# Performance work log

Hardware: AMD Instinct MI355X
Metric: run time of the kernel (lower is better)

The kernel has to match this reference:

```python
import jax, jax.numpy as jnp
import numpy as np

B = 64


def _upsample_conv1x1(f, cw, cb, size):
    # bilinear upsample (align_corners=False == jax half-pixel) + 1x1 conv
    u = jax.image.resize(f, (f.shape[0], f.shape[1], size, size), method='bilinear')
    return jnp.einsum('bchw,oc->bohw', u, cw) + cb[None, :, None, None]


def _shuffle_byblock(x, perms, block_size):
    # Rearrange 'b c (h h1) (w w1) -> b c (h w) h1 w1', then per-block channel
    # permutation: shuffled[:, j, i] = blocks[:, perms[i, j], i], then inverse.
    Bsz, C, H, _ = x.shape
    nb = H // block_size
    blocks = x.reshape(Bsz, C, nb, block_size, nb, block_size)
    blocks = blocks.transpose(0, 1, 2, 4, 3, 5).reshape(Bsz, C, nb * nb, block_size, block_size)
    idx = perms[: nb * nb].T  # [C, nb*nb]; idx[j, i] = perms[i, j]
    shuf = jnp.take_along_axis(blocks, idx[None, :, :, None, None], axis=1)
    shuf = shuf.reshape(Bsz, C, nb, nb, block_size, block_size)
    shuf = shuf.transpose(0, 1, 2, 4, 3, 5).reshape(Bsz, C, H, H)
    return shuf


def setup_inputs() -> dict:
    key = jax.random.key(0)
    ks = jax.random.split(key, 10)
    f1 = jax.random.normal(ks[0], (B, 64, 28, 28), jnp.float32)
    f2 = jax.random.normal(ks[1], (B, 128, 14, 14), jnp.float32)
    f3 = jax.random.normal(ks[2], (B, 128, 7, 7), jnp.float32)
    f4 = jax.random.normal(ks[3], (B, 512, 7, 7), jnp.float32)
    x_final = jax.random.normal(ks[4], (B, 512), jnp.float32)
    cw1 = jax.random.normal(ks[5], (64, 64), jnp.float32) * 0.1
    cb1 = jnp.zeros((64,), jnp.float32)
    cw2 = jax.random.normal(ks[6], (128, 128), jnp.float32) * 0.1
    cb2 = jnp.zeros((128,), jnp.float32)
    cw3 = jax.random.normal(ks[7], (256, 128), jnp.float32) * 0.1
    cb3 = jnp.zeros((256,), jnp.float32)
    cw4 = jax.random.normal(ks[8], (512, 512), jnp.float32) * 0.1
    cb4 = jnp.zeros((512,), jnp.float32)
    w1 = jnp.ones((64, 56, 56), jnp.float32)
    w2 = jnp.ones((128, 28, 28), jnp.float32)
    w3 = jnp.ones((256, 14, 14), jnp.float32)
    w4 = jnp.ones((512, 7, 7), jnp.float32)
    rng = np.random.default_rng(0)
    perms = jnp.asarray(np.stack([rng.permutation(64) for _ in range(28 * 28)]).astype(np.int32))
    return dict(f1=f1, f2=f2, f3=f3, f4=f4, x_final=x_final,
                cw1=cw1, cb1=cb1, cw2=cw2, cb2=cb2, cw3=cw3, cb3=cb3, cw4=cw4, cb4=cb4,
                w1=w1, w2=w2, w3=w3, w4=w4, perms=perms)


def reference(f1, f2, f3, f4, x_final, cw1, cb1, cw2, cb2, cw3, cb3, cw4, cb4,
              w1, w2, w3, w4, perms):
    aux1 = _shuffle_byblock(_upsample_conv1x1(f1, cw1, cb1, 56), perms, 28)
    aux2 = _upsample_conv1x1(f2, cw2, cb2, 28)
    aux3 = _upsample_conv1x1(f3, cw3, cb3, 14)
    aux4 = _upsample_conv1x1(f4, cw4, cb4, 7)
    return (x_final, aux1, aux2, aux3, aux4, w1, w2, w3, w4)
```

## Files before the change

### kernel.cpp

```cpp
#include <hip/hip_runtime.h>
#include <hip/hip_bf16.h>
#include <cstddef>

typedef __attribute__((ext_vector_type(8))) short bf16x8;
typedef __attribute__((ext_vector_type(4))) float f32x4;

__device__ __forceinline__ float4 ld4(const float* p) { return *(const float4*)p; }
__device__ __forceinline__ unsigned short f2bf(float v) {
  __hip_bfloat16 h = __float2bfloat16(v);
  return *(unsigned short*)&h;
}

__device__ __forceinline__ bf16x8 pack8(float v0, float v1, float v2, float v3,
                                        float v4, float v5, float v6, float v7) {
  bf16x8 r;
  r[0] = (short)f2bf(v0); r[1] = (short)f2bf(v1);
  r[2] = (short)f2bf(v2); r[3] = (short)f2bf(v3);
  r[4] = (short)f2bf(v4); r[5] = (short)f2bf(v5);
  r[6] = (short)f2bf(v6); r[7] = (short)f2bf(v7);
  return r;
}
__device__ __forceinline__ bf16x8 cfrag(const float* __restrict__ p) {
  float4 a = ld4(p), b = ld4(p + 4);
  return pack8(a.x, a.y, a.z, a.w, b.x, b.y, b.z, b.w);
}
__device__ __forceinline__ bf16x8 gfrag(const float* __restrict__ p, int stride) {
  float v0 = p[0], v1 = p[stride], v2 = p[2 * stride], v3 = p[3 * stride];
  float v4 = p[4 * stride], v5 = p[5 * stride], v6 = p[6 * stride], v7 = p[7 * stride];
  return pack8(v0, v1, v2, v3, v4, v5, v6, v7);
}
__device__ __forceinline__ bf16x8 gfrag_guard(const float* __restrict__ p, int stride, bool ok) {
  float v0 = ok ? p[0] : 0.f, v1 = ok ? p[stride] : 0.f;
  float v2 = ok ? p[2 * stride] : 0.f, v3 = ok ? p[3 * stride] : 0.f;
  float v4 = ok ? p[4 * stride] : 0.f, v5 = ok ? p[5 * stride] : 0.f;
  float v6 = ok ? p[6 * stride] : 0.f, v7 = ok ? p[7 * stride] : 0.f;
  return pack8(v0, v1, v2, v3, v4, v5, v6, v7);
}

__device__ __forceinline__ void up_quad_rows(const float* __restrict__ s0,
                                             const float* __restrict__ s1,
                                             const float* __restrict__ s2,
                                             int qx, int W, float* __restrict__ dst, int pitch) {
  int cm = qx > 0 ? qx - 1 : 0, cp = qx < W - 1 ? qx + 1 : W - 1;
  float tA0 = 0.25f * s0[cm] + 0.75f * s0[qx], tA1 = 0.75f * s0[qx] + 0.25f * s0[cp];
  float tB0 = 0.25f * s1[cm] + 0.75f * s1[qx], tB1 = 0.75f * s1[qx] + 0.25f * s1[cp];
  float tC0 = 0.25f * s2[cm] + 0.75f * s2[qx], tC1 = 0.75f * s2[qx] + 0.25f * s2[cp];
  *(float2*)dst = make_float2(0.25f * tA0 + 0.75f * tB0, 0.25f * tA1 + 0.75f * tB1);
  *(float2*)(dst + pitch) = make_float2(0.75f * tB0 + 0.25f * tC0, 0.75f * tB1 + 0.25f * tC1);
}

__device__ __forceinline__ void up_quad2(const float* __restrict__ s0,
                                         const float* __restrict__ s1,
                                         const float* __restrict__ s2,
                                         int qx0, int W, float* __restrict__ dst, int pitch) {
  int cm = qx0 > 0 ? qx0 - 1 : 0;
  int c2 = qx0 + 2 < W ? qx0 + 2 : W - 1;
  float Am = s0[cm], A0 = s0[qx0], A1 = s0[qx0 + 1], A2 = s0[c2];
  float Bm = s1[cm], B0 = s1[qx0], B1 = s1[qx0 + 1], B2 = s1[c2];
  float Cm = s2[cm], C0 = s2[qx0], C1 = s2[qx0 + 1], C2 = s2[c2];
  float hA0 = 0.25f * Am + 0.75f * A0, hA1 = 0.75f * A0 + 0.25f * A1;
  float hA2 = 0.25f * A0 + 0.75f * A1, hA3 = 0.75f * A1 + 0.25f * A2;
  float hB0 = 0.25f * Bm + 0.75f * B0, hB1 = 0.75f * B0 + 0.25f * B1;
  float hB2 = 0.25f * B0 + 0.75f * B1, hB3 = 0.75f * B1 + 0.25f * B2;
  float hC0 = 0.25f * Cm + 0.75f * C0, hC1 = 0.75f * C0 + 0.25f * C1;
  float hC2 = 0.25f * C0 + 0.75f * C1, hC3 = 0.75f * C1 + 0.25f * C2;
  *(float4*)dst = make_float4(0.25f * hA0 + 0.75f * hB0, 0.25f * hA1 + 0.75f * hB1,
                              0.25f * hA2 + 0.75f * hB2, 0.25f * hA3 + 0.75f * hB3);
  *(float4*)(dst + pitch) = make_float4(0.75f * hB0 + 0.25f * hC0, 0.75f * hB1 + 0.25f * hC1,
                                        0.75f * hB2 + 0.25f * hC2, 0.75f * hB3 + 0.25f * hC3);
}

struct P1M { float ct[16][252]; int inv[4][16]; };
struct C2M { float ct[32][126]; };
struct C3M { float ct[64][49]; };
union SmemM { P1M p1; C2M c2; C3M c3; };

__device__ __forceinline__ int2 xcd_decode(int d, int wpb_log) {
  int xcd = d & 7;
  int i = (d >> 3) & ((1 << wpb_log) - 1);
  int b = (((d >> (3 + wpb_log)) << 3) | xcd);
  return make_int2(b, i);
}

__global__ void __launch_bounds__(256)
fused_all(const float* __restrict__ f1, const float* __restrict__ f2,
          const float* __restrict__ f3, const float* __restrict__ f4,
          const float* __restrict__ cw1, const float* __restrict__ cb1,
          const float* __restrict__ cw2, const float* __restrict__ cb2,
          const float* __restrict__ cw3, const float* __restrict__ cb3,
          const float* __restrict__ cw4, const float* __restrict__ cb4,
          const float* __restrict__ xf, const float* __restrict__ w1,
          const float* __restrict__ w2, const float* __restrict__ w3,
          const float* __restrict__ w4s, const int* __restrict__ perms,
          float* __restrict__ out) {
  __shared__ SmemM sm;
  const int raw = blockIdx.x, tid = threadIdx.x;
  const int wave = tid >> 6, lane = tid & 63;
  const int l15 = lane & 15, lg = lane >> 4;
  float* o_aux1 = out + 32768;
  float* o_aux2 = o_aux1 + 12845056;
  float* o_aux3 = o_aux2 + 6422528;
  float* o_aux4 = o_aux3 + 3211264;

  if (raw < 512) {
    int2 bi = xcd_decode(raw, 3);
    const int b = bi.x;
    const int wm = bi.y * 64 + wave * 16;
    const float* f4b = f4 + (size_t)b * 25088;

    f32x4 acc[4];
    {
      float bv0 = cb4[wm + lg * 4 + 0], bv1 = cb4[wm + lg * 4 + 1];
      float bv2 = cb4[wm + lg * 4 + 2], bv3 = cb4[wm + lg * 4 + 3];
      for (int n = 0; n < 4; ++n) {
        acc[n][0] = bv0; acc[n][1] = bv1; acc[n][2] = bv2; acc[n][3] = bv3;
      }
    }
    const float* ap = cw4 + (size_t)(wm + l15) * 512 + lg * 8;
    int poff[4]; bool pok[4];
#pragma unroll
    for (int n = 0; n < 4; ++n) {
      int p = n * 16 + l15;
      pok[n] = p < 49;
      poff[n] = pok[n] ? p : 0;
    }
#pragma unroll 2
    for (int k0 = 0; k0 < 512; k0 += 32) {
      bf16x8 A = cfrag(ap + k0);
      const float* fb = f4b + (size_t)(k0 + lg * 8) * 49;
      bf16x8 B0 = gfrag_guard(fb + poff[0], 49, pok[0]);
      bf16x8 B1 = gfrag_guard(fb + poff[1], 49, pok[1]);
      bf16x8 B2 = gfrag_guard(fb + poff[2], 49, pok[2]);
      bf16x8 B3 = gfrag_guard(fb + poff[3], 49, pok[3]);
      acc[0] = __builtin_amdgcn_mfma_f32_16x16x32_bf16(A, B0, acc[0], 0, 0, 0);
      acc[1] = __builtin_amdgcn_mfma_f32_16x16x32_bf16(A, B1, acc[1], 0, 0, 0);
      acc[2] = __builtin_amdgcn_mfma_f32_16x16x32_bf16(A, B2, acc[2], 0, 0, 0);
      acc[3] = __builtin_amdgcn_mfma_f32_16x16x32_bf16(A, B3, acc[3], 0, 0, 0);
    }
    float* outb = o_aux4 + (size_t)b * 25088;
#pragma unroll
    for (int n = 0; n < 4; ++n) {
      int p = n * 16 + l15;
      if (p < 49) {
#pragma unroll
        for (int r = 0; r < 4; ++r) {
          int o = wm + lg * 4 + r;
          outb[(size_t)o * 49 + p] = acc[n][r];
        }
      }
    }
  } else if (raw < 1536) {
    int2 bi = xcd_decode(raw - 512, 4);
    const int b = bi.x;
    const int o0 = (bi.y >> 2) * 16;
    const int r0 = (bi.y & 3) * 7, base = r0 - 1;
    const float* f1b = f1 + (size_t)b * 50176;

    if (tid >= 128 && tid < 192) {
      int t2 = tid - 128;
      int i = t2 >> 4, cl = t2 & 15;
      int c = o0 + cl;
      int r = 0;
      for (int j = 0; j < 64; ++j)
        if (perms[i * 64 + j] == c) r = j;
      sm.p1.inv[i][cl] = r;
    }

    int off[4];
#pragma unroll
    for (int j = 0; j < 4; ++j) {
      int praw = wave * 64 + j * 16 + l15;
      int p = praw < 251 ? praw : 251;
      int lr = p / 28, x = p - lr * 28;
      int sr = base + lr;
      sr = sr < 0 ? 0 : (sr > 27 ? 27 : sr);
      off[j] = sr * 28 + x;
    }
    f32x4 acc[4];
    {
      float bv0 = cb1[o0 + lg * 4 + 0], bv1 = cb1[o0 + lg * 4 + 1];
      float bv2 = cb1[o0 + lg * 4 + 2], bv3 = cb1[o0 + lg * 4 + 3];
#pragma unroll
      for (int j = 0; j < 4; ++j) {
        acc[j][0] = bv0; acc[j][1] = bv1; acc[j][2] = bv2; acc[j][3] = bv3;
      }
    }
    const float* ap = cw1 + (size_t)(o0 + l15) * 64 + lg * 8;
#pragma unroll
    for (int ks = 0; ks < 2; ++ks) {
      bf16x8 A = cfrag(ap + ks * 32);
      const float* fb = f1b + (size_t)(ks * 32 + lg * 8) * 784;
#pragma unroll
      for (int j = 0; j < 4; ++j) {
        bf16x8 B = gfrag(fb + off[j], 784);
        acc[j] = __builtin_amdgcn_mfma_f32_16x16x32_bf16(A, B, acc[j], 0, 0, 0);
      }
    }
#pragma unroll
    for (int j = 0; j < 4; ++j) {
      int praw = wave * 64 + j * 16 + l15;
      if (praw < 252) {
#pragma unroll
        for (int r = 0; r < 4; ++r) sm.p1.ct[lg * 4 + r][praw] = acc[j][r];
      }
    }
    __syncthreads();

    const size_t obase = (size_t)b * 200704;
    for (int i = tid; i < 1568; i += 256) {
      int cl = i / 98;
      int rem = i - cl * 98;
      int ly = rem / 14, pr = rem - ly * 14;
      int qx0 = 2 * pr;
      int qy = r0 + ly;
      int lr = ly + 1;
      int qi = ((qy >= 14) ? 2 : 0) + ((qx0 >= 14) ? 1 : 0);
      int j = sm.p1.inv[qi][cl];
      float* dst = o_aux1 + obase + (size_t)j * 3136 + (size_t)(2 * qy) * 56 + 2 * qx0;
      up_quad2(&sm.p1.ct[cl][(lr - 1) * 28], &sm.p1.ct[cl][lr * 28],
               &sm.p1.ct[cl][(lr + 1) * 28], qx0, 28, dst, 56);
    }
  } else if (raw < 2048) {
    int2 bi = xcd_decode(raw - 1536, 3);
    const int b = bi.x;
    const int o0 = (bi.y >> 1) * 32;
    const int r0 = (bi.y & 1) * 7, base = r0 - 1;
    const int og = wave >> 1, nt = wave & 1;
    const int om = o0 + og * 16;
    const float* f2b = f2 + (size_t)b * 25088;

    int off[4];
#pragma unroll
    for (int j = 0; j < 4; ++j) {
      int praw = nt * 64 + j * 16 + l15;
      int p = praw < 125 ? praw : 125;
      int lr = p / 14, x = p - lr * 14;
      int sr = base + lr;
      sr = sr < 0 ? 0 : (sr > 13 ? 13 : sr);
      off[j] = sr * 14 + x;
    }
    f32x4 acc[4];
    {
      float bv0 = cb2[om + lg * 4 + 0], bv1 = cb2[om + lg * 4 + 1];
      float bv2 = cb2[om + lg * 4 + 2], bv3 = cb2[om + lg * 4 + 3];
#pragma unroll
      for (int j = 0; j < 4; ++j) {
        acc[j][0] = bv0; acc[j][1] = bv1; acc[j][2] = bv2; acc[j][3] = bv3;
      }
    }
    const float* ap = cw2 + (size_t)(om + l15) * 128 + lg * 8;
#pragma unroll
    for (int ks = 0; ks < 4; ++ks) {
      bf16x8 A = cfrag(ap + ks * 32);
      const float* fb = f2b + (size_t)(ks * 32 + lg * 8) * 196;
#pragma unroll
      for (int j = 0; j < 4; ++j) {
        bf16x8 B = gfrag(fb + off[j], 196);
        acc[j] = __builtin_amdgcn_mfma_f32_16x16x32_bf16(A, B, acc[j], 0, 0, 0);
      }
    }
#pragma unroll
    for (int j = 0; j < 4; ++j) {
      int praw = nt * 64 + j * 16 + l15;
      if (praw < 126) {
#pragma unroll
        for (int r = 0; r < 4; ++r) sm.c2.ct[og * 16 + lg * 4 + r][praw] = acc[j][r];
      }
    }
    __syncthreads();

    const size_t obase = (size_t)b * 100352;
    for (int i = tid; i < 1568; i += 256) {
      int cl = i / 49;
      int rem = i - cl * 49;
      int ly = rem / 7, pr = rem - ly * 7;
      int qx0 = 2 * pr;
      int qy = r0 + ly;
      int lr = ly + 1;
      float* dst = o_aux2 + obase + (size_t)(o0 + cl) * 784 + (size_t)(2 * qy) * 28 + 2 * qx0;
      up_quad2(&sm.c2.ct[cl][(lr - 1) * 14], &sm.c2.ct[cl][lr * 14],
               &sm.c2.ct[cl][(lr + 1) * 14], qx0, 14, dst, 28);
    }
  } else if (raw < 2304) {
    int2 bi = xcd_decode(raw - 2048, 2);
    const int b = bi.x;
    const int o0 = bi.y * 64;
    const int om = o0 + wave * 16;
    const float* f3b = f3 + (size_t)b * 6272;

    int poff[4]; bool pok[4];
#pragma unroll
    for (int j = 0; j < 4; ++j) {
      int p = j * 16 + l15;
      pok[j] = p < 49;
      poff[j] = pok[j] ? p : 0;
    }
    f32x4 acc[4];
    {
      float bv0 = cb3[om + lg * 4 + 0], bv1 = cb3[om + lg * 4 + 1];
      float bv2 = cb3[om + lg * 4 + 2], bv3 = cb3[om + lg * 4 + 3];
#pragma unroll
      for (int j = 0; j < 4; ++j) {
        acc[j][0] = bv0; acc[j][1] = bv1; acc[j][2] = bv2; acc[j][3] = bv3;
      }
    }
    const float* ap = cw3 + (size_t)(om + l15) * 128 + lg * 8;
#pragma unroll
    for (int ks = 0; ks < 4; ++ks) {
      bf16x8 A = cfrag(ap + ks * 32);
      const float* fb = f3b + (size_t)(ks * 32 + lg * 8) * 49;
#pragma unroll
      for (int j = 0; j < 4; ++j) {
        bf16x8 B = gfrag_guard(fb + poff[j], 49, pok[j]);
        acc[j] = __builtin_amdgcn_mfma_f32_16x16x32_bf16(A, B, acc[j], 0, 0, 0);
      }
    }
#pragma unroll
    for (int j = 0; j < 4; ++j) {
      int p = j * 16 + l15;
      if (p < 49) {
#pragma unroll
        for (int r = 0; r < 4; ++r) sm.c3.ct[wave * 16 + lg * 4 + r][p] = acc[j][r];
      }
    }
    __syncthreads();

    const size_t obase = (size_t)b * 50176;
    for (int i = tid; i < 64 * 49; i += 256) {
      int cl = i / 49;
      int q = i - cl * 49;
      int qy = q / 7, qx = q - qy * 7;
      int rm = qy > 0 ? qy - 1 : 0, rp = qy < 6 ? qy + 1 : 6;
      float* dst = o_aux3 + obase + (size_t)(o0 + cl) * 196 + (size_t)(2 * qy) * 14 + 2 * qx;
      up_quad_rows(&sm.c3.ct[cl][rm * 7], &sm.c3.ct[cl][qy * 7], &sm.c3.ct[cl][rp * 7],
                   qx, 7, dst, 14);
    }
  } else {
    int idx = (raw - 2304) * 256 + tid;
    const int stride = 64 * 256;
    float4* o4 = (float4*)out;
    const size_t W1 = 6029312;
    for (int i = idx; i < 8192; i += stride) o4[i] = ((const float4*)xf)[i];
    for (int i = idx; i < 50176; i += stride) o4[W1 + i] = ((const float4*)w1)[i];
    for (int i = idx; i < 25088; i += stride) o4[W1 + 50176 + i] = ((const float4*)w2)[i];
    for (int i = idx; i < 12544; i += stride) o4[W1 + 75264 + i] = ((const float4*)w3)[i];
    for (int i = idx; i < 6272; i += stride) o4[W1 + 87808 + i] = ((const float4*)w4s)[i];
  }
}

extern "C" void kernel_launch(void* const* d_in, const int* in_sizes, int n_in,
                              void* d_out, int out_size, void* d_ws, size_t ws_size,
                              hipStream_t stream) {
  const float* f1      = (const float*)d_in[0];
  const float* f2      = (const float*)d_in[1];
  const float* f3      = (const float*)d_in[2];
  const float* f4      = (const float*)d_in[3];
  const float* x_final = (const float*)d_in[4];
  const float* cw1     = (const float*)d_in[5];
  const float* cb1     = (const float*)d_in[6];
  const float* cw2     = (const float*)d_in[7];
  const float* cb2     = (const float*)d_in[8];
  const float* cw3     = (const float*)d_in[9];
  const float* cb3     = (const float*)d_in[10];
  const float* cw4     = (const float*)d_in[11];
  const float* cb4     = (const float*)d_in[12];
  const float* w1      = (const float*)d_in[13];
  const float* w2      = (const float*)d_in[14];
  const float* w3      = (const float*)d_in[15];
  const float* w4      = (const float*)d_in[16];
  const int*   perms   = (const int*)d_in[17];

  float* out = (float*)d_out;

  fused_all<<<2368, 256, 0, stream>>>(f1, f2, f3, f4, cw1, cb1, cw2, cb2,
                                      cw3, cb3, cw4, cb4, x_final, w1, w2, w3, w4,
                                      perms, out);
}
```

Before: 49.39 us.

## Enlarge output-channel tiles per block to reuse B fragments across more MFMAs

Each block now covers more output channels: aux4 blocks handle 256 channels with a 4x4 MFMA tile per wave, and aux1 and aux2 blocks handle twice as many channels with two A fragments per B fragment. The grid shrinks from 2368 to 1216 blocks. The aim is to cut redundant global loads and bf16 conversion of the activation fragments and to lower block scheduling overhead. In exchange there are more accumulator registers, larger shared memory, and fewer blocks for the aux4 path (128), which may leave CUs idle and lengthen the critical path.

Result: slower. 51.27 us (+3.8%).

```diff
diff --git a/kernel.cpp b/kernel.cpp
--- a/kernel.cpp
+++ b/kernel.cpp
@@ -70,8 +70,8 @@
                                         0.75f * hB2 + 0.25f * hC2, 0.75f * hB3 + 0.25f * hC3);
 }
 
-struct P1M { float ct[16][252]; int inv[4][16]; };
-struct C2M { float ct[32][126]; };
+struct P1M { float ct[32][252]; int inv[4][32]; };
+struct C2M { float ct[64][126]; };
 struct C3M { float ct[64][49]; };
 union SmemM { P1M p1; C2M c2; C3M c3; };
 
@@ -102,21 +102,22 @@
   float* o_aux3 = o_aux2 + 6422528;
   float* o_aux4 = o_aux3 + 3211264;
 
-  if (raw < 512) {
-    int2 bi = xcd_decode(raw, 3);
+  if (raw < 128) {
+    int2 bi = xcd_decode(raw, 1);
     const int b = bi.x;
-    const int wm = bi.y * 64 + wave * 16;
+    const int ob = bi.y * 256 + wave * 64;
     const float* f4b = f4 + (size_t)b * 25088;
 
-    f32x4 acc[4];
-    {
-      float bv0 = cb4[wm + lg * 4 + 0], bv1 = cb4[wm + lg * 4 + 1];
-      float bv2 = cb4[wm + lg * 4 + 2], bv3 = cb4[wm + lg * 4 + 3];
+    f32x4 acc[4][4];
+#pragma unroll
+    for (int mi = 0; mi < 4; ++mi) {
+      float bv0 = cb4[ob + mi * 16 + lg * 4 + 0], bv1 = cb4[ob + mi * 16 + lg * 4 + 1];
+      float bv2 = cb4[ob + mi * 16 + lg * 4 + 2], bv3 = cb4[ob + mi * 16 + lg * 4 + 3];
+#pragma unroll
       for (int n = 0; n < 4; ++n) {
-        acc[n][0] = bv0; acc[n][1] = bv1; acc[n][2] = bv2; acc[n][3] = bv3;
-      }
-    }
-    const float* ap = cw4 + (size_t)(wm + l15) * 512 + lg * 8;
+        acc[mi][n][0] = bv0; acc[mi][n][1] = bv1; acc[mi][n][2] = bv2; acc[mi][n][3] = bv3;
+      }
+    }
     int poff[4]; bool pok[4];
 #pragma unroll
     for (int n = 0; n < 4; ++n) {
@@ -124,41 +125,59 @@
       pok[n] = p < 49;
       poff[n] = pok[n] ? p : 0;
     }
-#pragma unroll 2
+#pragma unroll 1
     for (int k0 = 0; k0 < 512; k0 += 32) {
-      bf16x8 A = cfrag(ap + k0);
+      bf16x8 A0 = cfrag(cw4 + (size_t)(ob + 0 + l15) * 512 + k0 + lg * 8);
+      bf16x8 A1 = cfrag(cw4 + (size_t)(ob + 16 + l15) * 512 + k0 + lg * 8);
+      bf16x8 A2 = cfrag(cw4 + (size_t)(ob + 32 + l15) * 512 + k0 + lg * 8);
+      bf16x8 A3 = cfrag(cw4 + (size_t)(ob + 48 + l15) * 512 + k0 + lg * 8);
       const float* fb = f4b + (size_t)(k0 + lg * 8) * 49;
       bf16x8 B0 = gfrag_guard(fb + poff[0], 49, pok[0]);
       bf16x8 B1 = gfrag_guard(fb + poff[1], 49, pok[1]);
       bf16x8 B2 = gfrag_guard(fb + poff[2], 49, pok[2]);
       bf16x8 B3 = gfrag_guard(fb + poff[3], 49, pok[3]);
-      acc[0] = __builtin_amdgcn_mfma_f32_16x16x32_bf16(A, B0, acc[0], 0, 0, 0);
-      acc[1] = __builtin_amdgcn_mfma_f32_16x16x32_bf16(A, B1, acc[1], 0, 0, 0);
-      acc[2] = __builtin_amdgcn_mfma_f32_16x16x32_bf16(A, B2, acc[2], 0, 0, 0);
-      acc[3] = __builtin_amdgcn_mfma_f32_16x16x32_bf16(A, B3, acc[3], 0, 0, 0);
+      acc[0][0] = __builtin_amdgcn_mfma_f32_16x16x32_bf16(A0, B0, acc[0][0], 0, 0, 0);
+      acc[0][1] = __builtin_amdgcn_mfma_f32_16x16x32_bf16(A0, B1, acc[0][1], 0, 0, 0);
+      acc[0][2] = __builtin_amdgcn_mfma_f32_16x16x32_bf16(A0, B2, acc[0][2], 0, 0, 0);
+      acc[0][3] = __builtin_amdgcn_mfma_f32_16x16x32_bf16(A0, B3, acc[0][3], 0, 0, 0);
+      acc[1][0] = __builtin_amdgcn_mfma_f32_16x16x32_bf16(A1, B0, acc[1][0], 0, 0, 0);
+      acc[1][1] = __builtin_amdgcn_mfma_f32_16x16x32_bf16(A1, B1, acc[1][1], 0, 0, 0);
+      acc[1][2] = __builtin_amdgcn_mfma_f32_16x16x32_bf16(A1, B2, acc[1][2], 0, 0, 0);
+      acc[1][3] = __builtin_amdgcn_mfma_f32_16x16x32_bf16(A1, B3, acc[1][3], 0, 0, 0);
+      acc[2][0] = __builtin_amdgcn_mfma_f32_16x16x32_bf16(A2, B0, acc[2][0], 0, 0, 0);
+      acc[2][1] = __builtin_amdgcn_mfma_f32_16x16x32_bf16(A2, B1, acc[2][1], 0, 0, 0);
+      acc[2][2] = __builtin_amdgcn_mfma_f32_16x16x32_bf16(A2, B2, acc[2][2], 0, 0, 0);
+      acc[2][3] = __builtin_amdgcn_mfma_f32_16x16x32_bf16(A2, B3, acc[2][3], 0, 0, 0);
+      acc[3][0] = __builtin_amdgcn_mfma_f32_16x16x32_bf16(A3, B0, acc[3][0], 0, 0, 0);
+      acc[3][1] = __builtin_amdgcn_mfma_f32_16x16x32_bf16(A3, B1, acc[3][1], 0, 0, 0);
+      acc[3][2] = __builtin_amdgcn_mfma_f32_16x16x32_bf16(A3, B2, acc[3][2], 0, 0, 0);
+      acc[3][3] = __builtin_amdgcn_mfma_f32_16x16x32_bf16(A3, B3, acc[3][3], 0, 0, 0);
     }
     float* outb = o_aux4 + (size_t)b * 25088;
 #pragma unroll
-    for (int n = 0; n < 4; ++n) {
-      int p = n * 16 + l15;
-      if (p < 49) {
-#pragma unroll
-        for (int r = 0; r < 4; ++r) {
-          int o = wm + lg * 4 + r;
-          outb[(size_t)o * 49 + p] = acc[n][r];
+    for (int mi = 0; mi < 4; ++mi) {
+#pragma unroll
+      for (int n = 0; n < 4; ++n) {
+        int p = n * 16 + l15;
+        if (p < 49) {
+#pragma unroll
+          for (int r = 0; r < 4; ++r) {
+            int o = ob + mi * 16 + lg * 4 + r;
+            outb[(size_t)o * 49 + p] = acc[mi][n][r];
+          }
         }
       }
     }
-  } else if (raw < 1536) {
-    int2 bi = xcd_decode(raw - 512, 4);
+  } else if (raw < 640) {
+    int2 bi = xcd_decode(raw - 128, 3);
     const int b = bi.x;
-    const int o0 = (bi.y >> 2) * 16;
+    const int o0 = (bi.y >> 2) * 32;
     const int r0 = (bi.y & 3) * 7, base = r0 - 1;
     const float* f1b = f1 + (size_t)b * 50176;
 
-    if (tid >= 128 && tid < 192) {
+    if (tid >= 128) {
       int t2 = tid - 128;
-      int i = t2 >> 4, cl = t2 & 15;
+      int i = t2 >> 5, cl = t2 & 31;
       int c = o0 + cl;
       int r = 0;
       for (int j = 0; j < 64; ++j)
@@ -176,38 +195,42 @@
       sr = sr < 0 ? 0 : (sr > 27 ? 27 : sr);
       off[j] = sr * 28 + x;
     }
-    f32x4 acc[4];
-    {
-      float bv0 = cb1[o0 + lg * 4 + 0], bv1 = cb1[o0 + lg * 4 + 1];
-      float bv2 = cb1[o0 + lg * 4 + 2], bv3 = cb1[o0 + lg * 4 + 3];
-#pragma unroll
-      for (int j = 0; j < 4; ++j) {
-        acc[j][0] = bv0; acc[j][1] = bv1; acc[j][2] = bv2; acc[j][3] = bv3;
-      }
-    }
-    const float* ap = cw1 + (size_t)(o0 + l15) * 64 + lg * 8;
+    f32x4 acc[2][4];
+#pragma unroll
+    for (int mi = 0; mi < 2; ++mi) {
+      float bv0 = cb1[o0 + mi * 16 + lg * 4 + 0], bv1 = cb1[o0 + mi * 16 + lg * 4 + 1];
+      float bv2 = cb1[o0 + mi * 16 + lg * 4 + 2], bv3 = cb1[o0 + mi * 16 + lg * 4 + 3];
+#pragma unroll
+      for (int j = 0; j < 4; ++j) {
+        acc[mi][j][0] = bv0; acc[mi][j][1] = bv1; acc[mi][j][2] = bv2; acc[mi][j][3] = bv3;
+      }
+    }
 #pragma unroll
     for (int ks = 0; ks < 2; ++ks) {
-      bf16x8 A = cfrag(ap + ks * 32);
+      bf16x8 A0 = cfrag(cw1 + (size_t)(o0 + 0 + l15) * 64 + ks * 32 + lg * 8);
+      bf16x8 A1 = cfrag(cw1 + (size_t)(o0 + 16 + l15) * 64 + ks * 32 + lg * 8);
       const float* fb = f1b + (size_t)(ks * 32 + lg * 8) * 784;
 #pragma unroll
       for (int j = 0; j < 4; ++j) {
         bf16x8 B = gfrag(fb + off[j], 784);
-        acc[j] = __builtin_amdgcn_mfma_f32_16x16x32_bf16(A, B, acc[j], 0, 0, 0);
-      }
-    }
-#pragma unroll
-    for (int j = 0; j < 4; ++j) {
-      int praw = wave * 64 + j * 16 + l15;
-      if (praw < 252) {
-#pragma unroll
-        for (int r = 0; r < 4; ++r) sm.p1.ct[lg * 4 + r][praw] = acc[j][r];
-      }
-    }
+        acc[0][j] = __builtin_amdgcn_mfma_f32_16x16x32_bf16(A0, B, acc[0][j], 0, 0, 0);
+        acc[1][j] = __builtin_amdgcn_mfma_f32_16x16x32_bf16(A1, B, acc[1][j], 0, 0, 0);
+      }
+    }
+#pragma unroll
+    for (int mi = 0; mi < 2; ++mi)
+#pragma unroll
+      for (int j = 0; j < 4; ++j) {
+        int praw = wave * 64 + j * 16 + l15;
+        if (praw < 252) {
+#pragma unroll
+          for (int r = 0; r < 4; ++r) sm.p1.ct[mi * 16 + lg * 4 + r][praw] = acc[mi][j][r];
+        }
+      }
     __syncthreads();
 
     const size_t obase = (size_t)b * 200704;
-    for (int i = tid; i < 1568; i += 256) {
+    for (int i = tid; i < 3136; i += 256) {
       int cl = i / 98;
       int rem = i - cl * 98;
       int ly = rem / 14, pr = rem - ly * 14;
@@ -220,13 +243,13 @@
       up_quad2(&sm.p1.ct[cl][(lr - 1) * 28], &sm.p1.ct[cl][lr * 28],
                &sm.p1.ct[cl][(lr + 1) * 28], qx0, 28, dst, 56);
     }
-  } else if (raw < 2048) {
-    int2 bi = xcd_decode(raw - 1536, 3);
+  } else if (raw < 896) {
+    int2 bi = xcd_decode(raw - 640, 2);
     const int b = bi.x;
-    const int o0 = (bi.y >> 1) * 32;
+    const int o0 = (bi.y >> 1) * 64;
     const int r0 = (bi.y & 1) * 7, base = r0 - 1;
     const int og = wave >> 1, nt = wave & 1;
-    const int om = o0 + og * 16;
+    const int om = o0 + og * 32;
     const float* f2b = f2 + (size_t)b * 25088;
 
     int off[4];
@@ -239,38 +262,42 @@
       sr = sr < 0 ? 0 : (sr > 13 ? 13 : sr);
       off[j] = sr * 14 + x;
     }
-    f32x4 acc[4];
-    {
-      float bv0 = cb2[om + lg * 4 + 0], bv1 = cb2[om + lg * 4 + 1];
-      float bv2 = cb2[om + lg * 4 + 2], bv3 = cb2[om + lg * 4 + 3];
-#pragma unroll
-      for (int j = 0; j < 4; ++j) {
-        acc[j][0] = bv0; acc[j][1] = bv1; acc[j][2] = bv2; acc[j][3] = bv3;
-      }
-    }
-    const float* ap = cw2 + (size_t)(om + l15) * 128 + lg * 8;
+    f32x4 acc[2][4];
+#pragma unroll
+    for (int mi = 0; mi < 2; ++mi) {
+      float bv0 = cb2[om + mi * 16 + lg * 4 + 0], bv1 = cb2[om + mi * 16 + lg * 4 + 1];
+      float bv2 = cb2[om + mi * 16 + lg * 4 + 2], bv3 = cb2[om + mi * 16 + lg * 4 + 3];
+#pragma unroll
+      for (int j = 0; j < 4; ++j) {
+        acc[mi][j][0] = bv0; acc[mi][j][1] = bv1; acc[mi][j][2] = bv2; acc[mi][j][3] = bv3;
+      }
+    }
 #pragma unroll
     for (int ks = 0; ks < 4; ++ks) {
-      bf16x8 A = cfrag(ap + ks * 32);
+      bf16x8 A0 = cfrag(cw2 + (size_t)(om + 0 + l15) * 128 + ks * 32 + lg * 8);
+      bf16x8 A1 = cfrag(cw2 + (size_t)(om + 16 + l15) * 128 + ks * 32 + lg * 8);
       const float* fb = f2b + (size_t)(ks * 32 + lg * 8) * 196;
 #pragma unroll
       for (int j = 0; j < 4; ++j) {
         bf16x8 B = gfrag(fb + off[j], 196);
-        acc[j] = __builtin_amdgcn_mfma_f32_16x16x32_bf16(A, B, acc[j], 0, 0, 0);
-      }
-    }
-#pragma unroll
-    for (int j = 0; j < 4; ++j) {
-      int praw = nt * 64 + j * 16 + l15;
-      if (praw < 126) {
-#pragma unroll
-        for (int r = 0; r < 4; ++r) sm.c2.ct[og * 16 + lg * 4 + r][praw] = acc[j][r];
-      }
-    }
+        acc[0][j] = __builtin_amdgcn_mfma_f32_16x16x32_bf16(A0, B, acc[0][j], 0, 0, 0);
+        acc[1][j] = __builtin_amdgcn_mfma_f32_16x16x32_bf16(A1, B, acc[1][j], 0, 0, 0);
+      }
+    }
+#pragma unroll
+    for (int mi = 0; mi < 2; ++mi)
+#pragma unroll
+      for (int j = 0; j < 4; ++j) {
+        int praw = nt * 64 + j * 16 + l15;
+        if (praw < 126) {
+#pragma unroll
+          for (int r = 0; r < 4; ++r) sm.c2.ct[og * 32 + mi * 16 + lg * 4 + r][praw] = acc[mi][j][r];
+        }
+      }
     __syncthreads();
 
     const size_t obase = (size_t)b * 100352;
-    for (int i = tid; i < 1568; i += 256) {
+    for (int i = tid; i < 3136; i += 256) {
       int cl = i / 49;
       int rem = i - cl * 49;
       int ly = rem / 7, pr = rem - ly * 7;
@@ -281,8 +308,8 @@
       up_quad2(&sm.c2.ct[cl][(lr - 1) * 14], &sm.c2.ct[cl][lr * 14],
                &sm.c2.ct[cl][(lr + 1) * 14], qx0, 14, dst, 28);
     }
-  } else if (raw < 2304) {
-    int2 bi = xcd_decode(raw - 2048, 2);
+  } else if (raw < 1152) {
+    int2 bi = xcd_decode(raw - 896, 2);
     const int b = bi.x;
     const int o0 = bi.y * 64;
     const int om = o0 + wave * 16;
@@ -336,7 +363,7 @@
                    qx, 7, dst, 14);
     }
   } else {
-    int idx = (raw - 2304) * 256 + tid;
+    int idx = (raw - 1152) * 256 + tid;
     const int stride = 64 * 256;
     float4* o4 = (float4*)out;
     const size_t W1 = 6029312;
@@ -372,7 +399,7 @@
 
   float* out = (float*)d_out;
 
-  fused_all<<<2368, 256, 0, stream>>>(f1, f2, f3, f4, cw1, cb1, cw2, cb2,
+  fused_all<<<1216, 256, 0, stream>>>(f1, f2, f3, f4, cw1, cb1, cw2, cb2,
                                       cw3, cb3, cw4, cb4, x_final, w1, w2, w3, w4,
                                       perms, out);
 }
```
